# Performance work log

Measured on AMD Instinct MI355X. Metric: run time of the kernel, lower is better.

The kernel has to match this reference:

```python
import jax, jax.numpy as jnp
import numpy as np

B, T, E = 4, 2048, 1024
NH = 16            # num_heads
DH = E // NH       # per-head dim
NE = 2048          # num_experts = block_size (literal constructor wiring)
HID = NH           # expert hidden_dim = num_heads (literal constructor wiring)
EPS = 1e-5


def setup_inputs() -> dict:
    key = jax.random.key(0)
    ks = jax.random.split(key, 12)
    s = 0.02
    return {
        "x": jax.random.normal(ks[0], (B, T, E), jnp.float32),
        "ln1_g": jnp.ones((E,), jnp.float32),
        "ln1_b": jnp.zeros((E,), jnp.float32),
        "ln2_g": jnp.ones((E,), jnp.float32),
        "ln2_b": jnp.zeros((E,), jnp.float32),
        "qkv_w": jax.random.normal(ks[1], (E, 3 * E), jnp.float32) * s,
        "qkv_b": jnp.zeros((3 * E,), jnp.float32),
        "proj_w": jax.random.normal(ks[2], (E, E), jnp.float32) * s,
        "proj_b": jnp.zeros((E,), jnp.float32),
        "gate_w": jax.random.normal(ks[3], (E, NE), jnp.float32) * s,
        "gate_b": jnp.zeros((NE,), jnp.float32),
        "w1": jax.random.normal(ks[4], (NE, E, HID), jnp.float32) * s,
        "b1": jnp.zeros((NE, HID), jnp.float32),
        "w2": jax.random.normal(ks[5], (NE, HID, E), jnp.float32) * s,
        "b2": jnp.zeros((NE, E), jnp.float32),
    }


def _layernorm(x, g, b):
    mu = jnp.mean(x, axis=-1, keepdims=True)
    var = jnp.mean(jnp.square(x - mu), axis=-1, keepdims=True)
    return (x - mu) * jax.lax.rsqrt(var + EPS) * g + b


def _attention(h, qkv_w, qkv_b, proj_w, proj_b):
    qkv = h @ qkv_w + qkv_b                       # [B,T,3E]
    qkv = qkv.reshape(h.shape[0], h.shape[1], 3, NH, DH)
    q, k, v = qkv[:, :, 0], qkv[:, :, 1], qkv[:, :, 2]   # [B,T,NH,DH]
    scores = jnp.einsum('bqhd,bkhd->bhqk', q, k) * (DH ** -0.5)
    causal = jnp.tril(jnp.ones((h.shape[1], h.shape[1]), bool))
    scores = jnp.where(causal, scores, -jnp.inf)
    attn = jax.nn.softmax(scores, axis=-1)
    out = jnp.einsum('bhqk,bkhd->bqhd', attn, v).reshape(h.shape[0], h.shape[1], E)
    return out @ proj_w + proj_b


def _moe(h, gate_w, gate_b, w1, b1, w2, b2):
    # top-1 routing via argmax of gate softmax (== argmax of logits)
    logits = h @ gate_w + gate_b                  # [B,T,NE]
    idx = jnp.argmax(logits, axis=-1)             # [B,T]
    xf = h.reshape(-1, E)                         # [N,E]
    fidx = idx.reshape(-1)                        # [N]
    tw1 = w1[fidx]                                # [N,E,HID]
    tb1 = b1[fidx]                                # [N,HID]
    tw2 = w2[fidx]                                # [N,HID,E]
    tb2 = b2[fidx]                                # [N,E]
    hmid = jax.nn.gelu(jnp.einsum('ne,neh->nh', xf, tw1) + tb1, approximate=False)
    yf = jnp.einsum('nh,nhe->ne', hmid, tw2) + tb2
    return yf.reshape(h.shape)


def reference(x, ln1_g, ln1_b, ln2_g, ln2_b, qkv_w, qkv_b, proj_w, proj_b,
              gate_w, gate_b, w1, b1, w2, b2):
    x = x + _attention(_layernorm(x, ln1_g, ln1_b), qkv_w, qkv_b, proj_w, proj_b)
    x = x + _moe(_layernorm(x, ln2_g, ln2_b), gate_w, gate_b, w1, b1, w2, b2)
    return x
```

## Files before the change

kernel.cpp:

```cpp
#include <hip/hip_runtime.h>
#include <math.h>

#define TOKENS 8192
#define EDIM   1024
#define TSEQ   2048
#define NEXP   2048

typedef __attribute__((ext_vector_type(8))) short short8;
typedef __attribute__((ext_vector_type(4))) float f32x4;

__device__ __forceinline__ short f2bf(float f) {
  union { float f; unsigned u; } c; c.f = f;
  unsigned r = c.u + 0x7fffu + ((c.u >> 16) & 1u);
  return (short)(r >> 16);
}
__device__ __forceinline__ float bf2f(short h) {
  union { unsigned u; float f; } c; c.u = ((unsigned)(unsigned short)h) << 16;
  return c.f;
}
__device__ __forceinline__ void split3(float a, short& p0, short& p1, short& p2) {
  p0 = f2bf(a);
  float r = a - bf2f(p0);
  p1 = f2bf(r);
  p2 = f2bf(r - bf2f(p1));
}
__device__ __forceinline__ void split2(float a, short& p0, short& p1) {
  p0 = f2bf(a);
  p1 = f2bf(a - bf2f(p0));
}

__global__ __launch_bounds__(256) void ln_kernel(const float* __restrict__ x,
    const float* __restrict__ g, const float* __restrict__ b,
    short* __restrict__ obf, float* __restrict__ of32)
{
  const int row = blockIdx.x;
  const int t = threadIdx.x, lane = t & 63, w = t >> 6;
  const float4 v = ((const float4*)(x + (size_t)row * EDIM))[t];
  __shared__ float lds[4];
  float s = v.x + v.y + v.z + v.w;
  #pragma unroll
  for (int m = 32; m >= 1; m >>= 1) s += __shfl_xor(s, m);
  if (lane == 0) lds[w] = s;
  __syncthreads();
  const float mu = (lds[0] + lds[1] + lds[2] + lds[3]) * (1.f / EDIM);
  __syncthreads();
  const float d0 = v.x - mu, d1 = v.y - mu, d2 = v.z - mu, d3 = v.w - mu;
  float sq = d0 * d0 + d1 * d1 + d2 * d2 + d3 * d3;
  #pragma unroll
  for (int m = 32; m >= 1; m >>= 1) sq += __shfl_xor(sq, m);
  if (lane == 0) lds[w] = sq;
  __syncthreads();
  const float var = (lds[0] + lds[1] + lds[2] + lds[3]) * (1.f / EDIM);
  const float rstd = rsqrtf(var + 1e-5f);
  const float4 gg = ((const float4*)g)[t];
  const float4 bb = ((const float4*)b)[t];
  const float y0 = d0 * rstd * gg.x + bb.x;
  const float y1 = d1 * rstd * gg.y + bb.y;
  const float y2 = d2 * rstd * gg.z + bb.z;
  const float y3 = d3 * rstd * gg.w + bb.w;
  if (obf) {
    unsigned long long pk =
        (unsigned long long)(unsigned short)f2bf(y0)
      | ((unsigned long long)(unsigned short)f2bf(y1) << 16)
      | ((unsigned long long)(unsigned short)f2bf(y2) << 32)
      | ((unsigned long long)(unsigned short)f2bf(y3) << 48);
    *(unsigned long long*)(obf + (size_t)row * EDIM + t * 4) = pk;
  }
  ((float4*)(of32 + (size_t)row * EDIM))[t] = make_float4(y0, y1, y2, y3);
}

__global__ __launch_bounds__(256) void wsplit_kernel(const float* __restrict__ W,
    short* __restrict__ Wt, int K, int N)
{
  __shared__ float tile[32][33];
  const int n0 = blockIdx.x * 32, k0 = blockIdx.y * 32;
  const int tx = threadIdx.x & 31, ty = threadIdx.x >> 5;
  #pragma unroll
  for (int i = 0; i < 4; i++)
    tile[ty * 4 + i][tx] = W[(size_t)(k0 + ty * 4 + i) * N + n0 + tx];
  __syncthreads();
  const size_t PS = (size_t)N * K;
  #pragma unroll
  for (int i = 0; i < 4; i++) {
    short p0, p1, p2;
    split3(tile[tx][ty * 4 + i], p0, p1, p2);
    const size_t idx = (size_t)(n0 + ty * 4 + i) * K + k0 + tx;
    Wt[idx] = p0; Wt[PS + idx] = p1; Wt[2 * PS + idx] = p2;
  }
}

__global__ __launch_bounds__(256) void wconv_kernel(const float* __restrict__ W,
    short* __restrict__ Wt, int K, int N)
{
  __shared__ float tile[32][33];
  const int n0 = blockIdx.x * 32, k0 = blockIdx.y * 32;
  const int tx = threadIdx.x & 31, ty = threadIdx.x >> 5;
  #pragma unroll
  for (int i = 0; i < 4; i++)
    tile[ty * 4 + i][tx] = W[(size_t)(k0 + ty * 4 + i) * N + n0 + tx];
  __syncthreads();
  #pragma unroll
  for (int i = 0; i < 4; i++)
    Wt[(size_t)(n0 + ty * 4 + i) * K + k0 + tx] = f2bf(tile[tx][ty * 4 + i]);
}

__global__ __launch_bounds__(256) void asplit_kernel(const float* __restrict__ src,
    short* __restrict__ dst, size_t PS)
{
  const size_t g8 = ((size_t)blockIdx.x * 256 + threadIdx.x) * 8;
  float v[8];
  *(float4*)&v[0] = *(const float4*)(src + g8);
  *(float4*)&v[4] = *(const float4*)(src + g8 + 4);
  short pl[3][8];
  #pragma unroll
  for (int j = 0; j < 8; j++) split3(v[j], pl[0][j], pl[1][j], pl[2][j]);
  *(short8*)(dst + g8)          = *(short8*)&pl[0][0];
  *(short8*)(dst + PS + g8)     = *(short8*)&pl[1][0];
  *(short8*)(dst + 2 * PS + g8) = *(short8*)&pl[2][0];
}

__global__ __launch_bounds__(256) void ksplit_kernel(const float* __restrict__ qkvf,
    short* __restrict__ Kp)
{
  const size_t gid = (size_t)blockIdx.x * 256 + threadIdx.x;
  const int tok = (int)(gid >> 7);
  const int c = (int)(gid & 127) * 8;
  const float* src = qkvf + (size_t)tok * 3072 + 1024 + c;
  float v[8];
  *(float4*)&v[0] = *(const float4*)src;
  *(float4*)&v[4] = *(const float4*)(src + 4);
  short pl[3][8];
  #pragma unroll
  for (int j = 0; j < 8; j++) split3(v[j], pl[0][j], pl[1][j], pl[2][j]);
  const size_t PS = (size_t)TOKENS * EDIM;
  const size_t dst = (size_t)tok * EDIM + c;
  *(short8*)(Kp + dst)          = *(short8*)&pl[0][0];
  *(short8*)(Kp + PS + dst)     = *(short8*)&pl[1][0];
  *(short8*)(Kp + 2 * PS + dst) = *(short8*)&pl[2][0];
}

__global__ __launch_bounds__(256) void vtrans_kernel(const float* __restrict__ qkvf,
    short* __restrict__ Vt)
{
  __shared__ float tile[32][33];
  const int bh = blockIdx.x;
  const int b = bh >> 4, h = bh & 15;
  const int t0 = blockIdx.y * 32;
  const int d0 = blockIdx.z * 32;
  const int tx = threadIdx.x & 31, ty = threadIdx.x >> 5;
  #pragma unroll
  for (int i = 0; i < 4; i++)
    tile[ty * 4 + i][tx] =
        qkvf[(size_t)(b * TSEQ + t0 + ty * 4 + i) * 3072 + 2048 + h * 64 + d0 + tx];
  __syncthreads();
  const size_t PS = (size_t)64 * 64 * TSEQ;
  #pragma unroll
  for (int i = 0; i < 4; i++) {
    short p0, p1, p2;
    split3(tile[tx][ty * 4 + i], p0, p1, p2);
    const size_t idx = (size_t)(bh * 64 + d0 + ty * 4 + i) * TSEQ + t0 + tx;
    Vt[idx] = p0; Vt[PS + idx] = p1; Vt[2 * PS + idx] = p2;
  }
}

template<int ADD_RES>
__global__ __launch_bounds__(256) void gemm_hp(const short* __restrict__ Ap, size_t astride,
    const short* __restrict__ Bp, size_t bstride, const float* __restrict__ bias,
    const float* __restrict__ resid, float* __restrict__ outp,
    int M, int N, int K)
{
  __shared__ short As[3][128][40];
  __shared__ short Bs[3][128][40];
  const int m0 = blockIdx.y * 128, n0 = blockIdx.x * 128;
  const int t = threadIdx.x;
  const int lane = t & 63, w = t >> 6;
  const int wm = w >> 1, wn = w & 1;
  const int lo = lane & 15, hi = lane >> 4;
  const int srow = t >> 1, sc0 = (t & 1) * 16;
  f32x4 acc[4][4];
  #pragma unroll
  for (int i = 0; i < 4; i++)
    #pragma unroll
    for (int j = 0; j < 4; j++)
      acc[i][j] = (f32x4){0.f, 0.f, 0.f, 0.f};

  for (int k0 = 0; k0 < K; k0 += 32) {
    #pragma unroll
    for (int p = 0; p < 3; p++) {
      const short* ap = Ap + (size_t)p * astride + (size_t)(m0 + srow) * K + k0 + sc0;
      *(uint4*)&As[p][srow][sc0]     = *(const uint4*)ap;
      *(uint4*)&As[p][srow][sc0 + 8] = *(const uint4*)(ap + 8);
      const short* bp = Bp + (size_t)p * bstride + (size_t)(n0 + srow) * K + k0 + sc0;
      *(uint4*)&Bs[p][srow][sc0]     = *(const uint4*)bp;
      *(uint4*)&Bs[p][srow][sc0 + 8] = *(const uint4*)(bp + 8);
    }
    __syncthreads();
    short8 af[3][4], bf[3][4];
    #pragma unroll
    for (int p = 0; p < 3; p++)
      #pragma unroll
      for (int i = 0; i < 4; i++) {
        af[p][i] = *(const short8*)(&As[p][wm * 64 + i * 16 + lo][hi * 8]);
        bf[p][i] = *(const short8*)(&Bs[p][wn * 64 + i * 16 + lo][hi * 8]);
      }
    #pragma unroll
    for (int i = 0; i < 4; i++)
      #pragma unroll
      for (int j = 0; j < 4; j++) {
        acc[i][j] = __builtin_amdgcn_mfma_f32_16x16x32_bf16(af[0][i], bf[0][j], acc[i][j], 0, 0, 0);
        acc[i][j] = __builtin_amdgcn_mfma_f32_16x16x32_bf16(af[0][i], bf[1][j], acc[i][j], 0, 0, 0);
        acc[i][j] = __builtin_amdgcn_mfma_f32_16x16x32_bf16(af[1][i], bf[0][j], acc[i][j], 0, 0, 0);
        acc[i][j] = __builtin_amdgcn_mfma_f32_16x16x32_bf16(af[1][i], bf[1][j], acc[i][j], 0, 0, 0);
        acc[i][j] = __builtin_amdgcn_mfma_f32_16x16x32_bf16(af[0][i], bf[2][j], acc[i][j], 0, 0, 0);
        acc[i][j] = __builtin_amdgcn_mfma_f32_16x16x32_bf16(af[2][i], bf[0][j], acc[i][j], 0, 0, 0);
      }
    __syncthreads();
  }
  #pragma unroll
  for (int i = 0; i < 4; i++)
    #pragma unroll
    for (int j = 0; j < 4; j++)
      #pragma unroll
      for (int r = 0; r < 4; r++) {
        const int gm = m0 + wm * 64 + i * 16 + hi * 4 + r;
        const int gn = n0 + wn * 64 + j * 16 + lo;
        float v = acc[i][j][r] + bias[gn];
        if (ADD_RES) v += resid[(size_t)gm * N + gn];
        outp[(size_t)gm * N + gn] = v;
      }
}

__global__ __launch_bounds__(256) void attn_hp(const float* __restrict__ qkvf,
    const short* __restrict__ Kp, const short* __restrict__ Vt,
    float* __restrict__ attno)
{
  const int bh = blockIdx.x;
  const int b = bh >> 4, h = bh & 15;
  const int qb0 = blockIdx.y * 64;
  const int t = threadIdx.x, lane = t & 63, w = t >> 6;
  const int lo = lane & 15, hi = lane >> 4;
  __shared__ short Ks[3][32][72];
  __shared__ short Vs[3][64][40];
  __shared__ short Ps[2][4][16][40];
  const size_t base = (size_t)b * TSEQ * 3072;
  const size_t PSK = (size_t)TOKENS * EDIM;
  const size_t PSV = (size_t)64 * 64 * TSEQ;
  const int qw0 = qb0 + w * 16;
  short8 qf[3][2];
  #pragma unroll
  for (int c = 0; c < 2; c++) {
    const float* qp = qkvf + base + (size_t)(qw0 + lo) * 3072 + h * 64 + c * 32 + hi * 8;
    float qv[8];
    *(float4*)&qv[0] = *(const float4*)qp;
    *(float4*)&qv[4] = *(const float4*)(qp + 4);
    #pragma unroll
    for (int j = 0; j < 8; j++) {
      short s0, s1, s2;
      split3(qv[j] * 0.125f, s0, s1, s2);
      qf[0][c][j] = s0; qf[1][c][j] = s1; qf[2][c][j] = s2;
    }
  }
  float l_r[4] = {0.f, 0.f, 0.f, 0.f};
  f32x4 o[4];
  #pragma unroll
  for (int nb = 0; nb < 4; nb++) o[nb] = (f32x4){0.f, 0.f, 0.f, 0.f};

  const int key = t >> 3, c0 = (t & 7) * 8;
  const int dv = t >> 2, kc = (t & 3) * 8;
  const short* kbase = Kp + (size_t)(b * TSEQ + key) * EDIM + h * 64 + c0;
  const short* vbase = Vt + (size_t)(bh * 64 + dv) * TSEQ + kc;
  short8 kreg0 = *(const short8*)kbase;
  short8 kreg1 = *(const short8*)(kbase + PSK);
  short8 kreg2 = *(const short8*)(kbase + 2 * PSK);
  short8 vreg0 = *(const short8*)vbase;
  short8 vreg1 = *(const short8*)(vbase + PSV);
  short8 vreg2 = *(const short8*)(vbase + 2 * PSV);

  const int ntiles = 2 * blockIdx.y + 2;
  for (int tile = 0; tile < ntiles; tile++) {
    const int kt0 = tile * 32;
    __syncthreads();
    *(short8*)&Ks[0][key][c0] = kreg0;
    *(short8*)&Ks[1][key][c0] = kreg1;
    *(short8*)&Ks[2][key][c0] = kreg2;
    *(short8*)&Vs[0][dv][kc] = vreg0;
    *(short8*)&Vs[1][dv][kc] = vreg1;
    *(short8*)&Vs[2][dv][kc] = vreg2;
    __syncthreads();
    if (tile + 1 < ntiles) {
      const short* kp = kbase + (size_t)(tile + 1) * 32 * EDIM;
      const short* vp = vbase + (tile + 1) * 32;
      kreg0 = *(const short8*)kp;
      kreg1 = *(const short8*)(kp + PSK);
      kreg2 = *(const short8*)(kp + 2 * PSK);
      vreg0 = *(const short8*)vp;
      vreg1 = *(const short8*)(vp + PSV);
      vreg2 = *(const short8*)(vp + 2 * PSV);
    }
    if (kt0 <= qw0 + 15) {
      f32x4 s[2];
      __builtin_amdgcn_s_setprio(1);
      #pragma unroll
      for (int kb = 0; kb < 2; kb++) {
        f32x4 z = (f32x4){0.f, 0.f, 0.f, 0.f};
        #pragma unroll
        for (int c = 0; c < 2; c++) {
          const short8 kf0 = *(const short8*)(&Ks[0][kb * 16 + lo][c * 32 + hi * 8]);
          const short8 kf1 = *(const short8*)(&Ks[1][kb * 16 + lo][c * 32 + hi * 8]);
          const short8 kf2 = *(const short8*)(&Ks[2][kb * 16 + lo][c * 32 + hi * 8]);
          z = __builtin_amdgcn_mfma_f32_16x16x32_bf16(qf[0][c], kf0, z, 0, 0, 0);
          z = __builtin_amdgcn_mfma_f32_16x16x32_bf16(qf[0][c], kf1, z, 0, 0, 0);
          z = __builtin_amdgcn_mfma_f32_16x16x32_bf16(qf[1][c], kf0, z, 0, 0, 0);
          z = __builtin_amdgcn_mfma_f32_16x16x32_bf16(qf[1][c], kf1, z, 0, 0, 0);
          z = __builtin_amdgcn_mfma_f32_16x16x32_bf16(qf[0][c], kf2, z, 0, 0, 0);
          z = __builtin_amdgcn_mfma_f32_16x16x32_bf16(qf[2][c], kf0, z, 0, 0, 0);
        }
        s[kb] = z;
      }
      __builtin_amdgcn_s_setprio(0);
      #pragma unroll
      for (int r = 0; r < 4; r++) {
        const int qg = qw0 + hi * 4 + r;
        #pragma unroll
        for (int kb = 0; kb < 2; kb++) {
          const int kg = kt0 + kb * 16 + lo;
          float v = s[kb][r];
          v = (kg > qg) ? -1e30f : v;
          const float pv = __expf(v);
          s[kb][r] = pv;
          l_r[r] += pv;
        }
      }
      #pragma unroll
      for (int kb = 0; kb < 2; kb++)
        #pragma unroll
        for (int r = 0; r < 4; r++) {
          short p0, p1;
          split2(s[kb][r], p0, p1);
          Ps[0][w][hi * 4 + r][kb * 16 + lo] = p0;
          Ps[1][w][hi * 4 + r][kb * 16 + lo] = p1;
        }
      __threadfence_block();
      const short8 pf0 = *(const short8*)(&Ps[0][w][lo][hi * 8]);
      const short8 pf1 = *(const short8*)(&Ps[1][w][lo][hi * 8]);
      __builtin_amdgcn_s_setprio(1);
      #pragma unroll
      for (int nb = 0; nb < 4; nb++) {
        const short8 vb0 = *(const short8*)(&Vs[0][nb * 16 + lo][hi * 8]);
        const short8 vb1 = *(const short8*)(&Vs[1][nb * 16 + lo][hi * 8]);
        const short8 vb2 = *(const short8*)(&Vs[2][nb * 16 + lo][hi * 8]);
        o[nb] = __builtin_amdgcn_mfma_f32_16x16x32_bf16(pf0, vb0, o[nb], 0, 0, 0);
        o[nb] = __builtin_amdgcn_mfma_f32_16x16x32_bf16(pf0, vb1, o[nb], 0, 0, 0);
        o[nb] = __builtin_amdgcn_mfma_f32_16x16x32_bf16(pf1, vb0, o[nb], 0, 0, 0);
        o[nb] = __builtin_amdgcn_mfma_f32_16x16x32_bf16(pf1, vb1, o[nb], 0, 0, 0);
        o[nb] = __builtin_amdgcn_mfma_f32_16x16x32_bf16(pf0, vb2, o[nb], 0, 0, 0);
      }
      __builtin_amdgcn_s_setprio(0);
    }
  }
  #pragma unroll
  for (int r = 0; r < 4; r++)
    #pragma unroll
    for (int mm = 8; mm >= 1; mm >>= 1) l_r[r] += __shfl_xor(l_r[r], mm);
  #pragma unroll
  for (int nb = 0; nb < 4; nb++)
    #pragma unroll
    for (int r = 0; r < 4; r++) {
      const int tok = qw0 + hi * 4 + r;
      attno[(size_t)(b * TSEQ + tok) * EDIM + h * 64 + nb * 16 + lo] = o[nb][r] / l_r[r];
    }
}

__global__ __launch_bounds__(256) void gemm_bf16(const short* __restrict__ A,
    const short* __restrict__ Bt, const float* __restrict__ bias,
    float* __restrict__ outp, int M, int N, int K)
{
  __shared__ short As[128][72];
  __shared__ short Bs[128][72];
  const int m0 = blockIdx.y * 128, n0 = blockIdx.x * 128;
  const int t = threadIdx.x;
  const int lane = t & 63, w = t >> 6;
  const int wm = w >> 1, wn = w & 1;
  const int lo = lane & 15, hi = lane >> 4;
  f32x4 acc[4][4];
  #pragma unroll
  for (int i = 0; i < 4; i++)
    #pragma unroll
    for (int j = 0; j < 4; j++)
      acc[i][j] = (f32x4){0.f, 0.f, 0.f, 0.f};
  for (int k0 = 0; k0 < K; k0 += 64) {
    #pragma unroll
    for (int c = 0; c < 4; c++) {
      const int cc = t + 256 * c;
      const int row = cc >> 3, col = (cc & 7) * 8;
      *(uint4*)(&As[row][col]) = *(const uint4*)(A + (size_t)(m0 + row) * K + k0 + col);
      *(uint4*)(&Bs[row][col]) = *(const uint4*)(Bt + (size_t)(n0 + row) * K + k0 + col);
    }
    __syncthreads();
    #pragma unroll
    for (int kk = 0; kk < 2; kk++) {
      short8 af[4], bf[4];
      #pragma unroll
      for (int i = 0; i < 4; i++) {
        af[i] = *(const short8*)(&As[wm * 64 + i * 16 + lo][kk * 32 + hi * 8]);
        bf[i] = *(const short8*)(&Bs[wn * 64 + i * 16 + lo][kk * 32 + hi * 8]);
      }
      #pragma unroll
      for (int i = 0; i < 4; i++)
        #pragma unroll
        for (int j = 0; j < 4; j++)
          acc[i][j] = __builtin_amdgcn_mfma_f32_16x16x32_bf16(af[i], bf[j], acc[i][j], 0, 0, 0);
    }
    __syncthreads();
  }
  #pragma unroll
  for (int i = 0; i < 4; i++)
    #pragma unroll
    for (int j = 0; j < 4; j++)
      #pragma unroll
      for (int r = 0; r < 4; r++) {
        const int gm = m0 + wm * 64 + i * 16 + hi * 4 + r;
        const int gn = n0 + wn * 64 + j * 16 + lo;
        outp[(size_t)gm * N + gn] = acc[i][j][r] + bias[gn];
      }
}

__global__ __launch_bounds__(256) void gate_argmax(const float* __restrict__ logits,
    const float* __restrict__ h2f, const float* __restrict__ gw,
    const float* __restrict__ gb, int* __restrict__ eidx)
{
  const int token = blockIdx.x;
  const int t = threadIdx.x, lane = t & 63, w = t >> 6;
  const float* row = logits + (size_t)token * NEXP;
  float bm = -1e30f;
  #pragma unroll
  for (int c = 0; c < 8; c++) bm = fmaxf(bm, row[t + 256 * c]);
  #pragma unroll
  for (int m = 32; m >= 1; m >>= 1) bm = fmaxf(bm, __shfl_xor(bm, m));
  __shared__ float wred[4];
  __shared__ int cnt;
  __shared__ int cand[16];
  __shared__ float sred[4];
  if (t == 0) cnt = 0;
  if (lane == 0) wred[w] = bm;
  __syncthreads();
  const float maxv = fmaxf(fmaxf(wred[0], wred[1]), fmaxf(wred[2], wred[3]));
  const float thr = maxv - 0.03f;
  #pragma unroll
  for (int c = 0; c < 8; c++) {
    const int e = t + 256 * c;
    if (row[e] > thr) {
      const int p = atomicAdd(&cnt, 1);
      if (p < 16) cand[p] = e;
    }
  }
  __syncthreads();
  const int nc = cnt < 16 ? cnt : 16;
  if (nc == 1) {
    if (t == 0) eidx[token] = cand[0];
    return;
  }
  const float* xr = h2f + (size_t)token * EDIM;
  int best = NEXP; float bs = -1e30f;
  for (int c = 0; c < nc; c++) {
    const int e = cand[c];
    float p = 0.f;
    #pragma unroll
    for (int ii = 0; ii < 4; ii++) {
      const int i = t + 256 * ii;
      p += xr[i] * gw[(size_t)i * NEXP + e];
    }
    #pragma unroll
    for (int m = 32; m >= 1; m >>= 1) p += __shfl_xor(p, m);
    if (lane == 0) sred[w] = p;
    __syncthreads();
    const float s = sred[0] + sred[1] + sred[2] + sred[3] + gb[e];
    if (s > bs || (s == bs && e < best)) { bs = s; best = e; }
    __syncthreads();
  }
  if (t == 0) eidx[token] = best;
}

__global__ __launch_bounds__(256) void moe_kernel(const float* __restrict__ h2f,
    const int* __restrict__ eidx, const float* __restrict__ w1,
    const float* __restrict__ b1, const float* __restrict__ w2,
    const float* __restrict__ b2, float* __restrict__ out)
{
  const int token = blockIdx.x;
  const int t = threadIdx.x, lane = t & 63, w = t >> 6;
  const int e = eidx[token];
  const float* xr = h2f + (size_t)token * EDIM;
  const float* w1e = w1 + (size_t)e * (EDIM * 16);
  float acc[16];
  #pragma unroll
  for (int hh = 0; hh < 16; hh++) acc[hh] = 0.f;
  #pragma unroll
  for (int ii = 0; ii < 4; ii++) {
    const int i = t + 256 * ii;
    const float xi = xr[i];
    const float4* wr = (const float4*)(w1e + (size_t)i * 16);
    const float4 r0 = wr[0], r1 = wr[1], r2 = wr[2], r3 = wr[3];
    acc[0] = fmaf(xi, r0.x, acc[0]);  acc[1] = fmaf(xi, r0.y, acc[1]);
    acc[2] = fmaf(xi, r0.z, acc[2]);  acc[3] = fmaf(xi, r0.w, acc[3]);
    acc[4] = fmaf(xi, r1.x, acc[4]);  acc[5] = fmaf(xi, r1.y, acc[5]);
    acc[6] = fmaf(xi, r1.z, acc[6]);  acc[7] = fmaf(xi, r1.w, acc[7]);
    acc[8] = fmaf(xi, r2.x, acc[8]);  acc[9] = fmaf(xi, r2.y, acc[9]);
    acc[10] = fmaf(xi, r2.z, acc[10]); acc[11] = fmaf(xi, r2.w, acc[11]);
    acc[12] = fmaf(xi, r3.x, acc[12]); acc[13] = fmaf(xi, r3.y, acc[13]);
    acc[14] = fmaf(xi, r3.z, acc[14]); acc[15] = fmaf(xi, r3.w, acc[15]);
  }
  #pragma unroll
  for (int hh = 0; hh < 16; hh++)
    #pragma unroll
    for (int m = 32; m >= 1; m >>= 1) acc[hh] += __shfl_xor(acc[hh], m);
  __shared__ float red[4][16];
  __shared__ float hm[16];
  if (lane == 0) {
    #pragma unroll
    for (int hh = 0; hh < 16; hh++) red[w][hh] = acc[hh];
  }
  __syncthreads();
  if (t < 16) {
    const float s = red[0][t] + red[1][t] + red[2][t] + red[3][t] + b1[(size_t)e * 16 + t];
    hm[t] = 0.5f * s * (1.f + erff(s * 0.70710678118654752f));
  }
  __syncthreads();
  const float* w2e = w2 + (size_t)e * (16 * EDIM);
  float4 y = *(const float4*)(b2 + (size_t)e * EDIM + t * 4);
  const float4 res = *(const float4*)(out + (size_t)token * EDIM + t * 4);
  y.x += res.x; y.y += res.y; y.z += res.z; y.w += res.w;
  #pragma unroll
  for (int hh = 0; hh < 16; hh++) {
    const float hv = hm[hh];
    const float4 wv = *(const float4*)(w2e + (size_t)hh * EDIM + t * 4);
    y.x = fmaf(hv, wv.x, y.x);
    y.y = fmaf(hv, wv.y, y.y);
    y.z = fmaf(hv, wv.z, y.z);
    y.w = fmaf(hv, wv.w, y.w);
  }
  *(float4*)(out + (size_t)token * EDIM + t * 4) = y;
}

extern "C" void kernel_launch(void* const* d_in, const int* in_sizes, int n_in,
                              void* d_out, int out_size, void* d_ws, size_t ws_size,
                              hipStream_t stream) {
  const float* x      = (const float*)d_in[0];
  const float* ln1_g  = (const float*)d_in[1];
  const float* ln1_b  = (const float*)d_in[2];
  const float* ln2_g  = (const float*)d_in[3];
  const float* ln2_b  = (const float*)d_in[4];
  const float* qkv_w  = (const float*)d_in[5];
  const float* qkv_b  = (const float*)d_in[6];
  const float* proj_w = (const float*)d_in[7];
  const float* proj_b = (const float*)d_in[8];
  const float* gate_w = (const float*)d_in[9];
  const float* gate_b = (const float*)d_in[10];
  const float* w1     = (const float*)d_in[11];
  const float* b1     = (const float*)d_in[12];
  const float* w2     = (const float*)d_in[13];
  const float* b2     = (const float*)d_in[14];
  float* out = (float*)d_out;

  char* p = (char*)d_ws;
  short* wTq = (short*)p; p += 3ull * 3072 * 1024 * 2;
  short* wTp = (short*)p; p += 3ull * 1024 * 1024 * 2;
  short* wTg = (short*)p; p += 2048ull * 1024 * 2;
  short* h2  = (short*)p; p += (size_t)TOKENS * EDIM * 2;
  int* eidx  = (int*)p;   p += (size_t)TOKENS * 4;
  p = (char*)(((size_t)p + 255) & ~(size_t)255);
  float* R1  = (float*)p; p += (size_t)TOKENS * EDIM * 4;
  float* R2  = (float*)p; p += (size_t)TOKENS * 3072 * 4;
  short* Kp  = (short*)p; p += 3ull * TOKENS * EDIM * 2;
  short* Vt  = (short*)p; p += 3ull * 64 * 64 * TSEQ * 2;
  float* h1f = R1;
  float* attnof = R1;
  float* h2f = R1;
  float* qkvf = R2;
  float* logits = R2;
  const size_t PSA = (size_t)TOKENS * EDIM;

  wsplit_kernel<<<dim3(3072 / 32, 1024 / 32), 256, 0, stream>>>(qkv_w, wTq, 1024, 3072);
  wsplit_kernel<<<dim3(1024 / 32, 1024 / 32), 256, 0, stream>>>(proj_w, wTp, 1024, 1024);
  wconv_kernel<<<dim3(2048 / 32, 1024 / 32), 256, 0, stream>>>(gate_w, wTg, 1024, 2048);

  ln_kernel<<<TOKENS, 256, 0, stream>>>(x, ln1_g, ln1_b, nullptr, h1f);
  asplit_kernel<<<PSA / 8 / 256, 256, 0, stream>>>(h1f, Kp, PSA);
  gemm_hp<0><<<dim3(3072 / 128, TOKENS / 128), 256, 0, stream>>>(
      Kp, PSA, wTq, (size_t)3072 * 1024, qkv_b, nullptr, qkvf, TOKENS, 3072, 1024);
  ksplit_kernel<<<TOKENS * 128 / 256, 256, 0, stream>>>(qkvf, Kp);
  vtrans_kernel<<<dim3(64, TSEQ / 32, 2), 256, 0, stream>>>(qkvf, Vt);
  attn_hp<<<dim3(64, TSEQ / 64), 256, 0, stream>>>(qkvf, Kp, Vt, attnof);
  asplit_kernel<<<PSA / 8 / 256, 256, 0, stream>>>(attnof, Kp, PSA);
  gemm_hp<1><<<dim3(1024 / 128, TOKENS / 128), 256, 0, stream>>>(
      Kp, PSA, wTp, (size_t)1024 * 1024, proj_b, x, out, TOKENS, 1024, 1024);
  ln_kernel<<<TOKENS, 256, 0, stream>>>(out, ln2_g, ln2_b, h2, h2f);
  gemm_bf16<<<dim3(2048 / 128, TOKENS / 128), 256, 0, stream>>>(
      h2, wTg, gate_b, logits, TOKENS, 2048, 1024);
  gate_argmax<<<TOKENS, 256, 0, stream>>>(logits, h2f, gate_w, gate_b, eidx);
  moe_kernel<<<TOKENS, 256, 0, stream>>>(h2f, eidx, w1, b1, w2, b2, out);
}
```

Measured before the change: 1.287 ms.

## Prefetch next K-tile into registers and XOR-swizzle LDS in split-bf16 GEMM

The split-bf16 GEMM kernel now loads the next K slice from global memory into registers while the MFMA work for the current slice runs, then writes it to shared memory after a barrier. This hides global-load latency behind compute. The shared tiles drop their padding in favour of an XOR swizzle of 8-element chunks to avoid bank conflicts, and MFMA priority is raised with s_setprio. A min-occupancy hint of 3 blocks per SM is added, which risks register spills given the added prefetch registers.

```diff
diff --git a/kernel.cpp b/kernel.cpp
--- a/kernel.cpp
+++ b/kernel.cpp
@@ -164,19 +164,21 @@
 }
 
 template<int ADD_RES>
-__global__ __launch_bounds__(256) void gemm_hp(const short* __restrict__ Ap, size_t astride,
+__global__ __launch_bounds__(256, 3) void gemm_hp(const short* __restrict__ Ap, size_t astride,
     const short* __restrict__ Bp, size_t bstride, const float* __restrict__ bias,
     const float* __restrict__ resid, float* __restrict__ outp,
     int M, int N, int K)
 {
-  __shared__ short As[3][128][40];
-  __shared__ short Bs[3][128][40];
+  __shared__ short As[3][128][32];
+  __shared__ short Bs[3][128][32];
   const int m0 = blockIdx.y * 128, n0 = blockIdx.x * 128;
   const int t = threadIdx.x;
   const int lane = t & 63, w = t >> 6;
   const int wm = w >> 1, wn = w & 1;
   const int lo = lane & 15, hi = lane >> 4;
-  const int srow = t >> 1, sc0 = (t & 1) * 16;
+  const int rr = t >> 2;
+  const int wc8 = (((t & 3) ^ (rr & 3)) * 8);
+  const int rch = lo & 3;
   f32x4 acc[4][4];
   #pragma unroll
   for (int i = 0; i < 4; i++)
@@ -184,25 +186,48 @@
     for (int j = 0; j < 4; j++)
       acc[i][j] = (f32x4){0.f, 0.f, 0.f, 0.f};
 
+  const short* aptr = Ap + (size_t)(m0 + rr) * K + (t & 3) * 8;
+  const short* bptr = Bp + (size_t)(n0 + rr) * K + (t & 3) * 8;
+  uint4 areg[3][2], breg[3][2];
+
+  #pragma unroll
+  for (int p = 0; p < 3; p++)
+    #pragma unroll
+    for (int u = 0; u < 2; u++) {
+      areg[p][u] = *(const uint4*)(aptr + (size_t)p * astride + (size_t)u * 64 * K);
+      breg[p][u] = *(const uint4*)(bptr + (size_t)p * bstride + (size_t)u * 64 * K);
+    }
+  aptr += 32; bptr += 32;
+  #pragma unroll
+  for (int p = 0; p < 3; p++)
+    #pragma unroll
+    for (int u = 0; u < 2; u++) {
+      *(uint4*)&As[p][u * 64 + rr][wc8] = areg[p][u];
+      *(uint4*)&Bs[p][u * 64 + rr][wc8] = breg[p][u];
+    }
+  __syncthreads();
+
   for (int k0 = 0; k0 < K; k0 += 32) {
-    #pragma unroll
-    for (int p = 0; p < 3; p++) {
-      const short* ap = Ap + (size_t)p * astride + (size_t)(m0 + srow) * K + k0 + sc0;
-      *(uint4*)&As[p][srow][sc0]     = *(const uint4*)ap;
-      *(uint4*)&As[p][srow][sc0 + 8] = *(const uint4*)(ap + 8);
-      const short* bp = Bp + (size_t)p * bstride + (size_t)(n0 + srow) * K + k0 + sc0;
-      *(uint4*)&Bs[p][srow][sc0]     = *(const uint4*)bp;
-      *(uint4*)&Bs[p][srow][sc0 + 8] = *(const uint4*)(bp + 8);
-    }
-    __syncthreads();
     short8 af[3][4], bf[3][4];
     #pragma unroll
     for (int p = 0; p < 3; p++)
       #pragma unroll
       for (int i = 0; i < 4; i++) {
-        af[p][i] = *(const short8*)(&As[p][wm * 64 + i * 16 + lo][hi * 8]);
-        bf[p][i] = *(const short8*)(&Bs[p][wn * 64 + i * 16 + lo][hi * 8]);
-      }
+        af[p][i] = *(const short8*)(&As[p][wm * 64 + i * 16 + lo][(hi ^ rch) * 8]);
+        bf[p][i] = *(const short8*)(&Bs[p][wn * 64 + i * 16 + lo][(hi ^ rch) * 8]);
+      }
+    const int more = (k0 + 32 < K);
+    if (more) {
+      #pragma unroll
+      for (int p = 0; p < 3; p++)
+        #pragma unroll
+        for (int u = 0; u < 2; u++) {
+          areg[p][u] = *(const uint4*)(aptr + (size_t)p * astride + (size_t)u * 64 * K);
+          breg[p][u] = *(const uint4*)(bptr + (size_t)p * bstride + (size_t)u * 64 * K);
+        }
+      aptr += 32; bptr += 32;
+    }
+    __builtin_amdgcn_s_setprio(1);
     #pragma unroll
     for (int i = 0; i < 4; i++)
       #pragma unroll
@@ -214,7 +239,18 @@
         acc[i][j] = __builtin_amdgcn_mfma_f32_16x16x32_bf16(af[0][i], bf[2][j], acc[i][j], 0, 0, 0);
         acc[i][j] = __builtin_amdgcn_mfma_f32_16x16x32_bf16(af[2][i], bf[0][j], acc[i][j], 0, 0, 0);
       }
-    __syncthreads();
+    __builtin_amdgcn_s_setprio(0);
+    if (more) {
+      __syncthreads();
+      #pragma unroll
+      for (int p = 0; p < 3; p++)
+        #pragma unroll
+        for (int u = 0; u < 2; u++) {
+          *(uint4*)&As[p][u * 64 + rr][wc8] = areg[p][u];
+          *(uint4*)&Bs[p][u * 64 + rr][wc8] = breg[p][u];
+        }
+      __syncthreads();
+    }
   }
   #pragma unroll
   for (int i = 0; i < 4; i++)
```

Result: slower. 2.071 ms (+61.0%).
